# Kernel optimization log

Hardware: AMD Instinct MI355X
Metric: run time of the kernel (lower is better)

Reference implementation:

```python
import jax, jax.numpy as jnp
import numpy as np

# WeightOnlyInt8Linear forward: out = (x @ W_int8.astype(x.dtype).T) * scales
# NOTE: the original torch forward has a bug: when bias is not None it returns
# pre_bias (bias is never added), and when bias is None it would crash.
# Faithful math for a runnable configuration (bias=True) is therefore just
# the scaled matmul without bias.

IN_FEATURES = 4096
OUT_FEATURES = 16384
M = 256  # tokens


def setup_inputs() -> dict:
    key = jax.random.key(0)
    k1, k2, k3 = jax.random.split(key, 3)
    x = jax.random.normal(k1, (M, IN_FEATURES), dtype=jnp.float32)
    # int8 quantized weights in [-128, 127]
    weight = jax.random.randint(k2, (OUT_FEATURES, IN_FEATURES), -128, 128, dtype=jnp.int8)
    # per-output-channel dequant scales (positive, small)
    scales = jax.random.uniform(k3, (OUT_FEATURES,), dtype=jnp.float32, minval=0.001, maxval=0.02)
    return {"input": x, "weight": weight, "scales": scales}


def reference(input, weight, scales):
    # weight.to(input): upcast int8 -> activation dtype, then dense GEMM, then per-channel scale
    w = weight.astype(input.dtype)                      # [out, in]
    pre_bias = jnp.einsum('mk,nk->mn', input, w)        # [M, out]
    return pre_bias * scales                            # broadcast over out_features
```

## Files before the change

### kernel.cpp

```cpp
#include <hip/hip_runtime.h>
#include <stdint.h>

#define M_TOK 256
#define N_OUT 16384
#define K_IN  4096
#define BM 128
#define BN 128
#define BK 64
#define NSTEPS (K_IN / BK)

#define AS1 __attribute__((address_space(1)))
#define AS3 __attribute__((address_space(3)))

typedef short v8s __attribute__((ext_vector_type(8)));
typedef float v16f __attribute__((ext_vector_type(16)));
typedef int   v4i __attribute__((ext_vector_type(4)));
typedef unsigned int uint;

__device__ __forceinline__ unsigned short rne_bf16(float f) {
  uint u = __float_as_uint(f);
  uint r = u + 0x7FFFu + ((u >> 16) & 1u);
  return (unsigned short)(r >> 16);
}
__device__ __forceinline__ float bfbits_to_f(uint h) {
  return __uint_as_float(h << 16);
}

__global__ __launch_bounds__(256) void cast_kernel(
    const float* __restrict__ x, unsigned short* __restrict__ xhi,
    unsigned short* __restrict__ xlo) {
  const int i = (blockIdx.x * 256 + threadIdx.x) * 4;
  const float4 f = *(const float4*)(x + i);
  float fs[4] = {f.x, f.y, f.z, f.w};
  unsigned short h[4], l[4];
#pragma unroll
  for (int j = 0; j < 4; ++j) {
    h[j] = rne_bf16(fs[j]);
    l[j] = rne_bf16(fs[j] - bfbits_to_f(h[j]));
  }
  *(ushort4*)(xhi + i) = make_ushort4(h[0], h[1], h[2], h[3]);
  *(ushort4*)(xlo + i) = make_ushort4(l[0], l[1], l[2], l[3]);
}

__global__ __launch_bounds__(256, 1) void gemm_kernel(
    const unsigned short* __restrict__ xhi, const unsigned short* __restrict__ xlo,
    const void* __restrict__ wraw, const float* __restrict__ scales,
    float* __restrict__ out) {
  __shared__ alignas(16) unsigned char smem[98304];
  const int tid = threadIdx.x;
  const int lane = tid & 63;
  const int wid = tid >> 6;

  const int* wi = (const int*)wraw;
  const signed char* wb = (const signed char*)wraw;
  bool is32 = true;
#pragma unroll
  for (int i = 0; i < 16; ++i) {
    const int v = wi[i];
    is32 = is32 && (v >= -128) && (v <= 127);
  }

  const int bid = blockIdx.x;
  const int logical = (bid & 7) * 32 + (bid >> 3);
  const int mb = logical & 1;
  const int nb = logical >> 1;
  const int m0 = mb * BM;
  const int n0 = nb * BN;

  const int l8 = lane >> 3, e7 = lane & 7;
  const int cx = e7 ^ l8;
  size_t xoff[4];
  uint xdst[4];
#pragma unroll
  for (int j = 0; j < 4; ++j) {
    const int rw = wid * 4 + j;
    xoff[j] = (size_t)(m0 + rw * 8 + l8) * K_IN + (size_t)(cx * 8);
    xdst[j] = (uint)(rw * 1024);
  }

  const int wrow = tid >> 1, wh = tid & 1;
  const int* w32base = wi + (size_t)(n0 + wrow) * K_IN + wh * 32;
  const signed char* w8base = wb + (size_t)(n0 + wrow) * K_IN + wh * 32;
  uint wpos[4];
#pragma unroll
  for (int cc = 0; cc < 4; ++cc)
    wpos[cc] = 32768u + (uint)(wrow * 128) + (uint)((((4 * wh + cc) ^ (wrow & 7))) << 4);

  const int l31 = lane & 31, hi5 = lane >> 5;
  const int wm = (wid & 1) * 64, wn = (wid >> 1) * 64;
  uint arow[2], brow[2];
#pragma unroll
  for (int f = 0; f < 2; ++f) {
    arow[f] = (uint)((wm + f * 32 + l31) * 128);
    brow[f] = 32768u + (uint)((wn + f * 32 + l31) * 128);
  }

  v16f acc[2][2] = {};
  v4i wt[8];

  auto stage_tile = [&](int s, uint bo) {
#pragma unroll
    for (int j = 0; j < 4; ++j) {
      __builtin_amdgcn_global_load_lds(
          (const AS1 void*)(xhi + xoff[j] + (size_t)s * BK),
          (AS3 void*)(smem + bo + xdst[j]), 16, 0, 0);
      __builtin_amdgcn_global_load_lds(
          (const AS1 void*)(xlo + xoff[j] + (size_t)s * BK),
          (AS3 void*)(smem + bo + 16384 + xdst[j]), 16, 0, 0);
    }
    if (is32) {
#pragma unroll
      for (int i = 0; i < 8; ++i)
        wt[i] = *(const v4i*)(w32base + (size_t)s * BK + i * 4);
    } else {
      wt[0] = *(const v4i*)(w8base + (size_t)s * BK);
      wt[1] = *(const v4i*)(w8base + (size_t)s * BK + 16);
    }
  };

  auto conv_write_w = [&](uint bo) {
    int e[32];
    if (is32) {
#pragma unroll
      for (int i = 0; i < 8; ++i) {
        e[4 * i + 0] = wt[i].x; e[4 * i + 1] = wt[i].y;
        e[4 * i + 2] = wt[i].z; e[4 * i + 3] = wt[i].w;
      }
    } else {
      const signed char* bs = (const signed char*)wt;
#pragma unroll
      for (int j = 0; j < 32; ++j) e[j] = (int)bs[j];
    }
    uint d[16];
#pragma unroll
    for (int j = 0; j < 16; ++j)
      d[j] = (__float_as_uint((float)e[2 * j]) >> 16) |
             (__float_as_uint((float)e[2 * j + 1]) & 0xffff0000u);
#pragma unroll
    for (int cc = 0; cc < 4; ++cc) {
      v4i wv;
      wv.x = (int)d[4 * cc + 0]; wv.y = (int)d[4 * cc + 1];
      wv.z = (int)d[4 * cc + 2]; wv.w = (int)d[4 * cc + 3];
      *(v4i*)(smem + bo + wpos[cc]) = wv;
    }
  };

  stage_tile(0, 0u);
  conv_write_w(0u);
  __syncthreads();

  for (int t = 0; t < NSTEPS; ++t) {
    const uint bc = (t & 1) ? 49152u : 0u;
    const uint bn_ = bc ^ 49152u;
    const bool stagenext = (t + 1 < NSTEPS);
    if (stagenext) stage_tile(t + 1, bn_);
    __builtin_amdgcn_sched_barrier(0);

#pragma unroll
    for (int kc = 0; kc < 4; ++kc) {
      const uint pos = (uint)(((kc * 2 + hi5) ^ e7) << 4);
      v8s ah[2], al[2], b[2];
#pragma unroll
      for (int f = 0; f < 2; ++f) {
        ah[f] = *(const v8s*)(smem + bc + arow[f] + pos);
        al[f] = *(const v8s*)(smem + bc + 16384u + arow[f] + pos);
        b[f]  = *(const v8s*)(smem + bc + brow[f] + pos);
      }
#pragma unroll
      for (int mf = 0; mf < 2; ++mf)
#pragma unroll
        for (int nf = 0; nf < 2; ++nf) {
          acc[mf][nf] = __builtin_amdgcn_mfma_f32_32x32x16_bf16(ah[mf], b[nf], acc[mf][nf], 0, 0, 0);
          acc[mf][nf] = __builtin_amdgcn_mfma_f32_32x32x16_bf16(al[mf], b[nf], acc[mf][nf], 0, 0, 0);
        }
    }

    if (stagenext) conv_write_w(bn_);
    __syncthreads();
  }

#pragma unroll
  for (int nf = 0; nf < 2; ++nf) {
    const int n = n0 + wn + nf * 32 + l31;
    const float scl = scales[n];
#pragma unroll
    for (int mf = 0; mf < 2; ++mf)
#pragma unroll
      for (int reg = 0; reg < 16; ++reg) {
        const int m = m0 + wm + mf * 32 + (reg & 3) + 8 * (reg >> 2) + 4 * hi5;
        out[(size_t)m * N_OUT + n] = acc[mf][nf][reg] * scl;
      }
  }
}

__global__ void naive_kernel(const float* __restrict__ x, const void* __restrict__ wraw,
                             const float* __restrict__ scales, float* __restrict__ out) {
  const int* wi = (const int*)wraw;
  bool is32 = true;
  for (int i = 0; i < 16; ++i) { int v = wi[i]; is32 = is32 && v >= -128 && v <= 127; }
  const int idx = blockIdx.x * 256 + threadIdx.x;
  const int m = idx >> 14;
  const int n = idx & (N_OUT - 1);
  const float* xr = x + (size_t)m * K_IN;
  float acc = 0.f;
  if (is32) {
    const int* wr = wi + (size_t)n * K_IN;
    for (int k = 0; k < K_IN; ++k) acc += xr[k] * (float)wr[k];
  } else {
    const signed char* wr = (const signed char*)wraw + (size_t)n * K_IN;
    for (int k = 0; k < K_IN; ++k) acc += xr[k] * (float)wr[k];
  }
  out[idx] = acc * scales[n];
}

extern "C" void kernel_launch(void* const* d_in, const int* in_sizes, int n_in,
                              void* d_out, int out_size, void* d_ws, size_t ws_size,
                              hipStream_t stream) {
  const float* x = (const float*)d_in[0];
  const void* w = d_in[1];
  const float* scales = (const float*)d_in[2];
  float* out = (float*)d_out;
  if (ws_size >= (size_t)4 * 1024 * 1024) {
    unsigned short* xhi = (unsigned short*)d_ws;
    unsigned short* xlo = xhi + (size_t)M_TOK * K_IN;
    cast_kernel<<<(M_TOK * K_IN) / 1024, 256, 0, stream>>>(x, xhi, xlo);
    gemm_kernel<<<256, 256, 0, stream>>>(xhi, xlo, w, scales, out);
  } else {
    naive_kernel<<<(M_TOK * N_OUT) / 256, 256, 0, stream>>>(x, w, scales, out);
  }
}
```

Measured before the change: 470.4 us.

## Halve M tile, run two blocks per CU with new LDS layout

Cuts the block tile from 128x128 to 64x128, shrinks LDS to 64KB and sets launch bounds to two blocks per CU, launching 512 blocks instead of 256. The shared-memory layout for both activations and weights is redone: hi and lo halves are interleaved per row, weight rows are paired, and the XOR swizzle changes. The weight load mapping is also reworked so each thread reads 16-byte pieces spread over rows instead of contiguous spans of one row. The aim is more resident waves and better latency hiding on MI355X, at the cost of reading each weight tile twice as often, since four M blocks now share each N tile instead of two.

Measured after the change: 496.2 us. 1.06x slower.

```diff
diff --git a/kernel.cpp b/kernel.cpp
--- a/kernel.cpp
+++ b/kernel.cpp
@@ -4,7 +4,7 @@
 #define M_TOK 256
 #define N_OUT 16384
 #define K_IN  4096
-#define BM 128
+#define BM 64
 #define BN 128
 #define BK 64
 #define NSTEPS (K_IN / BK)
@@ -24,6 +24,9 @@
 }
 __device__ __forceinline__ float bfbits_to_f(uint h) {
   return __uint_as_float(h << 16);
+}
+__device__ __forceinline__ uint pack_bf16(float a, float b) {
+  return (__float_as_uint(a) >> 16) | (__float_as_uint(b) & 0xffff0000u);
 }
 
 __global__ __launch_bounds__(256) void cast_kernel(
@@ -42,11 +45,11 @@
   *(ushort4*)(xlo + i) = make_ushort4(l[0], l[1], l[2], l[3]);
 }
 
-__global__ __launch_bounds__(256, 1) void gemm_kernel(
+__global__ __launch_bounds__(256, 2) void gemm_kernel(
     const unsigned short* __restrict__ xhi, const unsigned short* __restrict__ xlo,
     const void* __restrict__ wraw, const float* __restrict__ scales,
     float* __restrict__ out) {
-  __shared__ alignas(16) unsigned char smem[98304];
+  __shared__ alignas(16) unsigned char smem[65536];
   const int tid = threadIdx.x;
   const int lane = tid & 63;
   const int wid = tid >> 6;
@@ -61,121 +64,127 @@
   }
 
   const int bid = blockIdx.x;
-  const int logical = (bid & 7) * 32 + (bid >> 3);
-  const int mb = logical & 1;
-  const int nb = logical >> 1;
+  const int logical = (bid & 7) * 64 + (bid >> 3);
+  const int mb = logical & 3;
+  const int nb = logical >> 2;
   const int m0 = mb * BM;
   const int n0 = nb * BN;
 
-  const int l8 = lane >> 3, e7 = lane & 7;
-  const int cx = e7 ^ l8;
-  size_t xoff[4];
+  const unsigned short* xsrc[4];
   uint xdst[4];
 #pragma unroll
   for (int j = 0; j < 4; ++j) {
-    const int rw = wid * 4 + j;
-    xoff[j] = (size_t)(m0 + rw * 8 + l8) * K_IN + (size_t)(cx * 8);
-    xdst[j] = (uint)(rw * 1024);
-  }
-
-  const int wrow = tid >> 1, wh = tid & 1;
-  const int* w32base = wi + (size_t)(n0 + wrow) * K_IN + wh * 32;
-  const signed char* w8base = wb + (size_t)(n0 + wrow) * K_IN + wh * 32;
-  uint wpos[4];
-#pragma unroll
-  for (int cc = 0; cc < 4; ++cc)
-    wpos[cc] = 32768u + (uint)(wrow * 128) + (uint)((((4 * wh + cc) ^ (wrow & 7))) << 4);
+    const int s = wid * 4 + j;
+    const int r = 4 * s + (lane >> 4);
+    const int c = (lane & 15) ^ (r & 15);
+    xsrc[j] = xhi + (size_t)(c >> 3) * M_TOK * K_IN
+            + (size_t)(m0 + r) * K_IN + (size_t)((c & 7) * 8);
+    xdst[j] = (uint)(s * 1024);
+  }
+
+  const int wr32 = tid >> 4, wc32 = tid & 15;
+  const int* w32base = wi + (size_t)(n0 + wr32) * K_IN + (size_t)(wc32 * 4);
+  const int wr8 = tid >> 2, wc8 = tid & 3;
+  const signed char* w8base = wb + (size_t)(n0 + wr8) * K_IN + (size_t)(wc8 * 16);
 
   const int l31 = lane & 31, hi5 = lane >> 5;
-  const int wm = (wid & 1) * 64, wn = (wid >> 1) * 64;
-  uint arow[2], brow[2];
-#pragma unroll
-  for (int f = 0; f < 2; ++f) {
-    arow[f] = (uint)((wm + f * 32 + l31) * 128);
-    brow[f] = 32768u + (uint)((wn + f * 32 + l31) * 128);
-  }
-
-  v16f acc[2][2] = {};
+  const int wm = (wid & 1) * 32;
+  const int wn = (wid >> 1) * 64;
+  const uint abase = (uint)((wm + l31) * 256);
+  const uint axor = (uint)((wm + l31) & 15);
+  uint bbase[2], bxor[2], bsel[2];
+#pragma unroll
+  for (int nf = 0; nf < 2; ++nf) {
+    const int wrow = wn + nf * 32 + l31;
+    const int q = wrow >> 1;
+    bbase[nf] = (uint)(q * 256);
+    bxor[nf] = (uint)(q & 15);
+    bsel[nf] = (uint)((wrow & 1) * 8);
+  }
+
+  v16f acc[2] = {};
   v4i wt[8];
 
-  auto stage_tile = [&](int s, uint bo) {
-#pragma unroll
-    for (int j = 0; j < 4; ++j) {
+  auto stage = [&](int s, uint xb) {
+#pragma unroll
+    for (int j = 0; j < 4; ++j)
       __builtin_amdgcn_global_load_lds(
-          (const AS1 void*)(xhi + xoff[j] + (size_t)s * BK),
-          (AS3 void*)(smem + bo + xdst[j]), 16, 0, 0);
-      __builtin_amdgcn_global_load_lds(
-          (const AS1 void*)(xlo + xoff[j] + (size_t)s * BK),
-          (AS3 void*)(smem + bo + 16384 + xdst[j]), 16, 0, 0);
-    }
+          (const AS1 void*)(xsrc[j] + (size_t)s * BK),
+          (AS3 void*)(smem + xb + xdst[j]), 16, 0, 0);
     if (is32) {
 #pragma unroll
       for (int i = 0; i < 8; ++i)
-        wt[i] = *(const v4i*)(w32base + (size_t)s * BK + i * 4);
+        wt[i] = *(const v4i*)(w32base + (size_t)i * 16 * K_IN + (size_t)s * 64);
     } else {
-      wt[0] = *(const v4i*)(w8base + (size_t)s * BK);
-      wt[1] = *(const v4i*)(w8base + (size_t)s * BK + 16);
+#pragma unroll
+      for (int i = 0; i < 2; ++i)
+        wt[i] = *(const v4i*)(w8base + (size_t)i * 64 * K_IN + (size_t)s * 64);
     }
   };
 
-  auto conv_write_w = [&](uint bo) {
-    int e[32];
+  auto conv_write_w = [&](uint wo) {
     if (is32) {
 #pragma unroll
       for (int i = 0; i < 8; ++i) {
-        e[4 * i + 0] = wt[i].x; e[4 * i + 1] = wt[i].y;
-        e[4 * i + 2] = wt[i].z; e[4 * i + 3] = wt[i].w;
+        const int r = i * 16 + wr32;
+        const int q = r >> 1;
+        const int chunk = (r & 1) * 8 + (wc32 >> 1);
+        const uint byte = wo + (uint)(q * 256) + (uint)((chunk ^ (q & 15)) << 4) +
+                          (uint)((wc32 & 1) * 8);
+        uint2 d;
+        d.x = pack_bf16((float)wt[i].x, (float)wt[i].y);
+        d.y = pack_bf16((float)wt[i].z, (float)wt[i].w);
+        *(uint2*)(smem + byte) = d;
       }
     } else {
-      const signed char* bs = (const signed char*)wt;
-#pragma unroll
-      for (int j = 0; j < 32; ++j) e[j] = (int)bs[j];
-    }
-    uint d[16];
-#pragma unroll
-    for (int j = 0; j < 16; ++j)
-      d[j] = (__float_as_uint((float)e[2 * j]) >> 16) |
-             (__float_as_uint((float)e[2 * j + 1]) & 0xffff0000u);
-#pragma unroll
-    for (int cc = 0; cc < 4; ++cc) {
-      v4i wv;
-      wv.x = (int)d[4 * cc + 0]; wv.y = (int)d[4 * cc + 1];
-      wv.z = (int)d[4 * cc + 2]; wv.w = (int)d[4 * cc + 3];
-      *(v4i*)(smem + bo + wpos[cc]) = wv;
+#pragma unroll
+      for (int i = 0; i < 2; ++i) {
+        const int r = i * 64 + wr8;
+        const int q = r >> 1;
+        const signed char* bs = (const signed char*)&wt[i];
+        uint u[4];
+#pragma unroll
+        for (int p = 0; p < 4; ++p)
+          u[p] = pack_bf16((float)bs[2 * p], (float)bs[2 * p + 1]);
+        uint u2[4];
+#pragma unroll
+        for (int p = 0; p < 4; ++p)
+          u2[p] = pack_bf16((float)bs[8 + 2 * p], (float)bs[8 + 2 * p + 1]);
+        const int cb = (r & 1) * 8 + wc8 * 2;
+        const uint b0 = wo + (uint)(q * 256) + (uint)(((cb + 0) ^ (q & 15)) << 4);
+        const uint b1 = wo + (uint)(q * 256) + (uint)(((cb + 1) ^ (q & 15)) << 4);
+        *(v4i*)(smem + b0) = *(v4i*)&u[0];
+        *(v4i*)(smem + b1) = *(v4i*)&u2[0];
+      }
     }
   };
 
-  stage_tile(0, 0u);
-  conv_write_w(0u);
+  stage(0, 0u);
+  conv_write_w(32768u);
   __syncthreads();
 
   for (int t = 0; t < NSTEPS; ++t) {
-    const uint bc = (t & 1) ? 49152u : 0u;
-    const uint bn_ = bc ^ 49152u;
-    const bool stagenext = (t + 1 < NSTEPS);
-    if (stagenext) stage_tile(t + 1, bn_);
+    const uint cur = (uint)(t & 1) << 14;
+    const uint xb = cur, wo = 32768u + cur;
+    const uint nxb = xb ^ 16384u, nwo = wo ^ 16384u;
+    const bool more = (t + 1 < NSTEPS);
+    if (more) stage(t + 1, nxb);
     __builtin_amdgcn_sched_barrier(0);
 
 #pragma unroll
     for (int kc = 0; kc < 4; ++kc) {
-      const uint pos = (uint)(((kc * 2 + hi5) ^ e7) << 4);
-      v8s ah[2], al[2], b[2];
-#pragma unroll
-      for (int f = 0; f < 2; ++f) {
-        ah[f] = *(const v8s*)(smem + bc + arow[f] + pos);
-        al[f] = *(const v8s*)(smem + bc + 16384u + arow[f] + pos);
-        b[f]  = *(const v8s*)(smem + bc + brow[f] + pos);
-      }
-#pragma unroll
-      for (int mf = 0; mf < 2; ++mf)
-#pragma unroll
-        for (int nf = 0; nf < 2; ++nf) {
-          acc[mf][nf] = __builtin_amdgcn_mfma_f32_32x32x16_bf16(ah[mf], b[nf], acc[mf][nf], 0, 0, 0);
-          acc[mf][nf] = __builtin_amdgcn_mfma_f32_32x32x16_bf16(al[mf], b[nf], acc[mf][nf], 0, 0, 0);
-        }
-    }
-
-    if (stagenext) conv_write_w(bn_);
+      const uint ch = (uint)(kc * 2 + hi5);
+      v8s ah = *(const v8s*)(smem + xb + abase + ((ch ^ axor) << 4));
+      v8s al = *(const v8s*)(smem + xb + abase + (((ch + 8u) ^ axor) << 4));
+      v8s b0 = *(const v8s*)(smem + wo + bbase[0] + (((bsel[0] + ch) ^ bxor[0]) << 4));
+      v8s b1 = *(const v8s*)(smem + wo + bbase[1] + (((bsel[1] + ch) ^ bxor[1]) << 4));
+      acc[0] = __builtin_amdgcn_mfma_f32_32x32x16_bf16(ah, b0, acc[0], 0, 0, 0);
+      acc[0] = __builtin_amdgcn_mfma_f32_32x32x16_bf16(al, b0, acc[0], 0, 0, 0);
+      acc[1] = __builtin_amdgcn_mfma_f32_32x32x16_bf16(ah, b1, acc[1], 0, 0, 0);
+      acc[1] = __builtin_amdgcn_mfma_f32_32x32x16_bf16(al, b1, acc[1], 0, 0, 0);
+    }
+
+    if (more) conv_write_w(nwo);
     __syncthreads();
   }
 
@@ -184,12 +193,10 @@
     const int n = n0 + wn + nf * 32 + l31;
     const float scl = scales[n];
 #pragma unroll
-    for (int mf = 0; mf < 2; ++mf)
-#pragma unroll
-      for (int reg = 0; reg < 16; ++reg) {
-        const int m = m0 + wm + mf * 32 + (reg & 3) + 8 * (reg >> 2) + 4 * hi5;
-        out[(size_t)m * N_OUT + n] = acc[mf][nf][reg] * scl;
-      }
+    for (int reg = 0; reg < 16; ++reg) {
+      const int m = m0 + wm + (reg & 3) + 8 * (reg >> 2) + 4 * hi5;
+      out[(size_t)m * N_OUT + n] = acc[nf][reg] * scl;
+    }
   }
 }
 
@@ -224,7 +231,7 @@
     unsigned short* xhi = (unsigned short*)d_ws;
     unsigned short* xlo = xhi + (size_t)M_TOK * K_IN;
     cast_kernel<<<(M_TOK * K_IN) / 1024, 256, 0, stream>>>(x, xhi, xlo);
-    gemm_kernel<<<256, 256, 0, stream>>>(xhi, xlo, w, scales, out);
+    gemm_kernel<<<512, 256, 0, stream>>>(xhi, xlo, w, scales, out);
   } else {
     naive_kernel<<<(M_TOK * N_OUT) / 256, 256, 0, stream>>>(x, w, scales, out);
   }
```
